# Kernel tuning notes

Measured on AMD Instinct MI355X. Metric: run time of the kernel, lower is better.

## Reference

```python
import jax, jax.numpy as jnp
import numpy as np

D = 512      # dgm / hidden width
L = 3        # n_dgm_layers
B = 131072   # collocation batch
SCALE = 0.02 # init scale to keep gates unsaturated


def setup_inputs() -> dict:
    key = jax.random.key(0)
    ks = jax.random.split(key, 12)
    X = jax.random.normal(ks[0], (B, 2), jnp.float32)
    t = jax.random.uniform(ks[1], (B, 1), jnp.float32)
    # input layer: Linear(3, D)
    W_in = jax.random.normal(ks[2], (3, D), jnp.float32) * SCALE
    b_in = jnp.zeros((D,), jnp.float32)
    # dense hidden: Linear(D, D)
    W_h1 = jax.random.normal(ks[3], (D, D), jnp.float32) * SCALE
    b_h1 = jnp.zeros((D,), jnp.float32)
    # projection to dgm dims: Linear(D, D)
    W_hd = jax.random.normal(ks[4], (D, D), jnp.float32) * SCALE
    b_hd = jnp.zeros((D,), jnp.float32)
    # DGM layers: 12 linears each, order [Uz,Wz,Bz, Ug,Wg,Bg, Ur,Wr,Br, Uh,Wh,Bh]
    dgm_W = jax.random.normal(ks[5], (L, 12, D, D), jnp.float32) * SCALE
    dgm_b = jnp.zeros((L, 12, D), jnp.float32)
    # output head: Linear(D, 1)
    W_out = jax.random.normal(ks[6], (D, 1), jnp.float32) * SCALE
    b_out = jnp.zeros((1,), jnp.float32)
    return {"X": X, "t": t, "W_in": W_in, "b_in": b_in, "W_h1": W_h1,
            "b_h1": b_h1, "W_hd": W_hd, "b_hd": b_hd, "dgm_W": dgm_W,
            "dgm_b": dgm_b, "W_out": W_out, "b_out": b_out}


def reference(X, t, W_in, b_in, W_h1, b_h1, W_hd, b_hd, dgm_W, dgm_b, W_out, b_out):
    inp = jnp.concatenate([X, t], axis=1)          # [B, 3]
    x = jnp.tanh(inp @ W_in + b_in)                # input layer + tanh
    x = jnp.tanh(x @ W_h1 + b_h1)                  # hidden Linear + tanh
    x = x @ W_hd + b_hd                            # hidden -> dgm projection (no act)
    S1 = x
    S = x
    for l in range(L):                             # small fixed layer loop
        W = dgm_W[l]
        b = dgm_b[l]
        lin = lambda i, v: v @ W[i] + b[i]
        Z = jax.nn.sigmoid(lin(0, x) + lin(1, S) + lin(2, S1))
        G = jax.nn.sigmoid(lin(3, x) + lin(4, S1) + lin(5, S))
        R = jax.nn.sigmoid(lin(6, x) + lin(7, S) + lin(8, S1))
        H = jnp.tanh(lin(9, x) + lin(10, S * R) + lin(11, S1))
        S = (1.0 - G) * H + Z * S
    return S @ W_out + b_out                       # [B, 1]
```

## Files before the change

### kernel.cpp

```cpp
#include <hip/hip_runtime.h>
#include <stdint.h>

namespace {

constexpr int B_ROWS = 131072;

typedef __attribute__((ext_vector_type(8))) short bf16x8;
typedef __attribute__((ext_vector_type(4))) float f32x4;

__device__ __forceinline__ unsigned short f2bf(float f) {
  unsigned u = __builtin_bit_cast(unsigned, f);
  u += 0x7fffu + ((u >> 16) & 1u);
  return (unsigned short)(u >> 16);
}
__device__ __forceinline__ float bf2f(unsigned short h) {
  unsigned u = ((unsigned)h) << 16;
  return __builtin_bit_cast(float, u);
}
__device__ __forceinline__ float sigm(float v) { return 1.0f / (1.0f + __expf(-v)); }


__global__ void pack_t_k(const float* __restrict__ W, unsigned short* __restrict__ Wt) {
  int idx = blockIdx.x * 256 + threadIdx.x;
  int n = idx >> 9, k = idx & 511;
  Wt[idx] = f2bf(W[(k << 9) + n]);
}

__global__ void pack_zgr_k(const float* __restrict__ dgmW, unsigned short* __restrict__ Wt) {
  long idx = (long)blockIdx.x * 256 + threadIdx.x;
  int l = (int)(idx / (1536 * 1024));
  int rest = (int)(idx - (long)l * (1536 * 1024));
  int n = rest >> 10, k = rest & 1023;
  int g = n >> 9, nn = n & 511;
  const int xi0[3] = {0, 3, 6};
  const int xi1[3] = {2, 4, 8};
  const int si[3] = {1, 5, 7};
  float v;
  if (k < 512)
    v = dgmW[(((long)(l * 12 + xi0[g]) << 9) + k) * 512 + nn] +
        dgmW[(((long)(l * 12 + xi1[g]) << 9) + k) * 512 + nn];
  else
    v = dgmW[(((long)(l * 12 + si[g]) << 9) + (k - 512)) * 512 + nn];
  Wt[idx] = f2bf(v);
}

__global__ void pack_h_k(const float* __restrict__ dgmW, unsigned short* __restrict__ Wt) {
  long idx = (long)blockIdx.x * 256 + threadIdx.x;
  int l = (int)(idx / (512 * 1024));
  int rest = (int)(idx - (long)l * (512 * 1024));
  int n = rest >> 10, k = rest & 1023;
  float v;
  if (k < 512)
    v = dgmW[(((long)(l * 12 + 9) << 9) + k) * 512 + n] +
        dgmW[(((long)(l * 12 + 11) << 9) + k) * 512 + n];
  else
    v = dgmW[(((long)(l * 12 + 10) << 9) + (k - 512)) * 512 + n];
  Wt[idx] = f2bf(v);
}

__global__ void pack_bias_k(const float* __restrict__ dgmb, float* __restrict__ bzgr,
                            float* __restrict__ bh) {
  int idx = blockIdx.x * 256 + threadIdx.x;
  if (idx >= 3 * 2048) return;
  int l = idx >> 11, n = idx & 2047;
  const float* bl = dgmb + l * 12 * 512;
  if (n < 1536) {
    int g = n >> 9, nn = n & 511;
    bzgr[l * 1536 + n] =
        bl[(g * 3 + 0) * 512 + nn] + bl[(g * 3 + 1) * 512 + nn] + bl[(g * 3 + 2) * 512 + nn];
  } else {
    int nn = n - 1536;
    bh[l * 512 + nn] = bl[9 * 512 + nn] + bl[10 * 512 + nn] + bl[11 * 512 + nn];
  }
}

__global__ void front0_k(const float* __restrict__ X, const float* __restrict__ t,
                         const float* __restrict__ Win, const float* __restrict__ bin,
                         unsigned short* __restrict__ x0, long row0) {
  long idx = (long)blockIdx.x * 256 + threadIdx.x;
  long r = idx >> 9;
  int c = (int)(idx & 511);
  long gr = row0 + r;
  float a = X[gr * 2] * Win[c] + X[gr * 2 + 1] * Win[512 + c] + t[gr] * Win[1024 + c] + bin[c];
  x0[idx] = f2bf(tanhf(a));
}

__global__ void head_k(const unsigned short* __restrict__ S, const float* __restrict__ Wout,
                       const float* __restrict__ bout, float* __restrict__ out, long row0) {
  const int lane = threadIdx.x & 63, wid = threadIdx.x >> 6;
  const long r = (long)blockIdx.x * 4 + wid;
  bf16x8 sv = *(const bf16x8*)&S[r * 512 + lane * 8];
  float sum = 0.f;
#pragma unroll
  for (int i = 0; i < 8; ++i) sum += bf2f((unsigned short)sv[i]) * Wout[lane * 8 + i];
#pragma unroll
  for (int off = 32; off > 0; off >>= 1) sum += __shfl_down(sum, off);
  if (lane == 0) out[row0 + r] = sum + bout[0];
}

template <int EPI, int KTILES>
__global__ __launch_bounds__(256, 2) void gemm_k(
    const unsigned short* __restrict__ a0, const unsigned short* __restrict__ a1,
    const unsigned short* __restrict__ wt, const float* __restrict__ bias,
    unsigned short* __restrict__ o0, unsigned short* __restrict__ o1,
    unsigned short* __restrict__ o2, const unsigned short* __restrict__ e0,
    const unsigned short* __restrict__ e1) {
  constexpr int K = KTILES * 64;
  __shared__ __align__(16) unsigned short As[128 * 64];
  __shared__ __align__(16) unsigned short Bs[128 * 64];
  const int tid = threadIdx.x;
  const int lane = tid & 63;
  const int wid = tid >> 6;
  const int wm = wid >> 1, wn = wid & 1;
  const long brow = (long)blockIdx.y * 128;
  const int bcol = blockIdx.x * 128;
  f32x4 acc[4][4] = {};

  for (int kt = 0; kt < KTILES; ++kt) {
    const unsigned short* asrc = (kt < 8) ? a0 : a1;
    const int kloc = (kt & 7) * 64;
    __syncthreads();
#pragma unroll
    for (int i = 0; i < 4; ++i) {
      const int c = tid + 256 * i;
      const int r = c >> 3, k8 = (c & 7) * 8;
      __builtin_amdgcn_global_load_lds(
          (const __attribute__((address_space(1))) void*)(asrc + (brow + r) * 512 + kloc + k8),
          (__attribute__((address_space(3))) void*)(&As[c * 8]), 16, 0, 0);
      __builtin_amdgcn_global_load_lds(
          (const __attribute__((address_space(1))) void*)(wt + (long)(bcol + r) * K + kt * 64 + k8),
          (__attribute__((address_space(3))) void*)(&Bs[c * 8]), 16, 0, 0);
    }
    __syncthreads();
#pragma unroll
    for (int ks = 0; ks < 2; ++ks) {
      bf16x8 af[4], bfv[4];
#pragma unroll
      for (int m = 0; m < 4; ++m)
        af[m] = *(const bf16x8*)&As[(wm * 64 + m * 16 + (lane & 15)) * 64 + ks * 32 + (lane >> 4) * 8];
#pragma unroll
      for (int n = 0; n < 4; ++n)
        bfv[n] = *(const bf16x8*)&Bs[(wn * 64 + n * 16 + (lane & 15)) * 64 + ks * 32 + (lane >> 4) * 8];
#pragma unroll
      for (int m = 0; m < 4; ++m)
#pragma unroll
        for (int n = 0; n < 4; ++n)
          acc[m][n] = __builtin_amdgcn_mfma_f32_16x16x32_bf16(af[m], bfv[n], acc[m][n], 0, 0, 0);
    }
  }

  const int g = bcol >> 9;
#pragma unroll
  for (int m = 0; m < 4; ++m) {
#pragma unroll
    for (int n = 0; n < 4; ++n) {
      const int col = bcol + wn * 64 + n * 16 + (lane & 15);
      const float bs = bias[col];
#pragma unroll
      for (int j = 0; j < 4; ++j) {
        const long row = brow + wm * 64 + m * 16 + (lane >> 4) * 4 + j;
        float v = acc[m][n][j] + bs;
        if constexpr (EPI == 0) {
          o0[row * 512 + col] = f2bf(tanhf(v));
        } else if constexpr (EPI == 1) {
          unsigned short b = f2bf(v);
          o0[row * 512 + col] = b;
          o1[row * 512 + col] = b;
        } else if constexpr (EPI == 2) {
          const int nn = col & 511;
          const float sgv = sigm(v);
          if (g == 0) {
            o0[row * 512 + nn] = f2bf(sgv * bf2f(e0[row * 512 + nn]));
          } else if (g == 1) {
            o1[row * 512 + nn] = f2bf(1.0f - sgv);
          } else {
            o2[row * 512 + nn] = f2bf(sgv * bf2f(e0[row * 512 + nn]));
          }
        } else {
          const float h = tanhf(v);
          const float omg = bf2f(e0[row * 512 + col]);
          const float zs = bf2f(e1[row * 512 + col]);
          o0[row * 512 + col] = f2bf(omg * h + zs);
        }
      }
    }
  }
}

}

extern "C" void kernel_launch(void* const* d_in, const int* in_sizes, int n_in,
                              void* d_out, int out_size, void* d_ws, size_t ws_size,
                              hipStream_t stream) {
  const float* X = (const float*)d_in[0];
  const float* t = (const float*)d_in[1];
  const float* W_in = (const float*)d_in[2];
  const float* b_in = (const float*)d_in[3];
  const float* W_h1 = (const float*)d_in[4];
  const float* b_h1 = (const float*)d_in[5];
  const float* W_hd = (const float*)d_in[6];
  const float* b_hd = (const float*)d_in[7];
  const float* dgm_W = (const float*)d_in[8];
  const float* dgm_b = (const float*)d_in[9];
  const float* W_out = (const float*)d_in[10];
  const float* b_out = (const float*)d_in[11];
  float* out = (float*)d_out;
  char* ws = (char*)d_ws;

  size_t off = 0;
  auto alloc = [&](size_t bytes) {
    size_t o = off;
    off = (off + bytes + 255) & ~(size_t)255;
    return o;
  };
  size_t o_wth1 = alloc((size_t)512 * 512 * 2);
  size_t o_wthd = alloc((size_t)512 * 512 * 2);
  size_t o_wtzgr = alloc((size_t)3 * 1536 * 1024 * 2);
  size_t o_wth = alloc((size_t)3 * 512 * 1024 * 2);
  size_t o_bzgr = alloc((size_t)3 * 1536 * 4);
  size_t o_bh = alloc((size_t)3 * 512 * 4);
  size_t actoff = off;

  unsigned short* wth1 = (unsigned short*)(ws + o_wth1);
  unsigned short* wthd = (unsigned short*)(ws + o_wthd);
  unsigned short* wtzgr = (unsigned short*)(ws + o_wtzgr);
  unsigned short* wth = (unsigned short*)(ws + o_wth);
  float* bzgr = (float*)(ws + o_bzgr);
  float* bh = (float*)(ws + o_bh);

  size_t avail = ws_size > actoff ? ws_size - actoff : 0;
  int nch = 1;
  while (nch < 1024 && (size_t)(B_ROWS / nch) * 512 * 2 * 5 > avail) nch <<= 1;
  const int R = B_ROWS / nch;
  unsigned short* xb = (unsigned short*)(ws + actoff);
  unsigned short* Sb = xb + (size_t)R * 512;
  unsigned short* ZSb = Sb + (size_t)R * 512;
  unsigned short* OGb = ZSb + (size_t)R * 512;
  unsigned short* SRb = OGb + (size_t)R * 512;

  pack_t_k<<<1024, 256, 0, stream>>>(W_h1, wth1);
  pack_t_k<<<1024, 256, 0, stream>>>(W_hd, wthd);
  pack_zgr_k<<<18432, 256, 0, stream>>>(dgm_W, wtzgr);
  pack_h_k<<<6144, 256, 0, stream>>>(dgm_W, wth);
  pack_bias_k<<<24, 256, 0, stream>>>(dgm_b, bzgr, bh);

  for (int c = 0; c < nch; ++c) {
    long row0 = (long)c * R;
    dim3 g4(4, R / 128), g12(12, R / 128);
    front0_k<<<R * 2, 256, 0, stream>>>(X, t, W_in, b_in, ZSb, row0);
    gemm_k<0, 8><<<g4, 256, 0, stream>>>(ZSb, nullptr, wth1, b_h1, OGb, nullptr, nullptr,
                                         nullptr, nullptr);
    gemm_k<1, 8><<<g4, 256, 0, stream>>>(OGb, nullptr, wthd, b_hd, xb, Sb, nullptr,
                                         nullptr, nullptr);
    for (int l = 0; l < 3; ++l) {
      gemm_k<2, 16><<<g12, 256, 0, stream>>>(xb, Sb, wtzgr + (size_t)l * 1536 * 1024,
                                             bzgr + l * 1536, ZSb, OGb, SRb, Sb, nullptr);
      gemm_k<3, 16><<<g4, 256, 0, stream>>>(xb, SRb, wth + (size_t)l * 512 * 1024,
                                            bh + l * 512, Sb, nullptr, nullptr, OGb, ZSb);
    }
    head_k<<<R / 4, 256, 0, stream>>>(Sb, W_out, b_out, out, row0);
  }
}
```

Baseline: 3.627 ms.

## Replace GEMM with 256x256-tile, 8-wave double-buffered pipelined kernel with XCD remap

Rewrites the bf16 MFMA GEMM to use 256x256 output tiles with 512 threads and 128KB of dynamic LDS, double-buffered across k-tiles. Loads are split into half-k stages and interleaved with the MFMA quarters, with explicit barriers, waitcnts and setprio. It adds an XOR swizzle on the LDS layout to avoid bank conflicts and remaps workgroups so each XCD gets contiguous tiles. The goal is more reuse per loaded byte and hiding global-load latency. The cost is fewer workgroups, higher register pressure from 32 accumulators per lane, and fragile hand scheduling.

```diff
diff --git a/kernel.cpp b/kernel.cpp
--- a/kernel.cpp
+++ b/kernel.cpp
@@ -99,66 +99,154 @@
 }
 
 template <int EPI, int KTILES>
-__global__ __launch_bounds__(256, 2) void gemm_k(
+__global__ __launch_bounds__(512, 2) void gemm8_k(
     const unsigned short* __restrict__ a0, const unsigned short* __restrict__ a1,
     const unsigned short* __restrict__ wt, const float* __restrict__ bias,
     unsigned short* __restrict__ o0, unsigned short* __restrict__ o1,
     unsigned short* __restrict__ o2, const unsigned short* __restrict__ e0,
     const unsigned short* __restrict__ e1) {
   constexpr int K = KTILES * 64;
-  __shared__ __align__(16) unsigned short As[128 * 64];
-  __shared__ __align__(16) unsigned short Bs[128 * 64];
+  constexpr int NT = KTILES;
+  extern __shared__ unsigned short lds[];
   const int tid = threadIdx.x;
   const int lane = tid & 63;
   const int wid = tid >> 6;
-  const int wm = wid >> 1, wn = wid & 1;
-  const long brow = (long)blockIdx.y * 128;
-  const int bcol = blockIdx.x * 128;
-  f32x4 acc[4][4] = {};
-
-  for (int kt = 0; kt < KTILES; ++kt) {
-    const unsigned short* asrc = (kt < 8) ? a0 : a1;
-    const int kloc = (kt & 7) * 64;
-    __syncthreads();
-#pragma unroll
-    for (int i = 0; i < 4; ++i) {
-      const int c = tid + 256 * i;
-      const int r = c >> 3, k8 = (c & 7) * 8;
-      __builtin_amdgcn_global_load_lds(
-          (const __attribute__((address_space(1))) void*)(asrc + (brow + r) * 512 + kloc + k8),
-          (__attribute__((address_space(3))) void*)(&As[c * 8]), 16, 0, 0);
-      __builtin_amdgcn_global_load_lds(
-          (const __attribute__((address_space(1))) void*)(wt + (long)(bcol + r) * K + kt * 64 + k8),
-          (__attribute__((address_space(3))) void*)(&Bs[c * 8]), 16, 0, 0);
-    }
-    __syncthreads();
-#pragma unroll
-    for (int ks = 0; ks < 2; ++ks) {
-      bf16x8 af[4], bfv[4];
-#pragma unroll
-      for (int m = 0; m < 4; ++m)
-        af[m] = *(const bf16x8*)&As[(wm * 64 + m * 16 + (lane & 15)) * 64 + ks * 32 + (lane >> 4) * 8];
-#pragma unroll
-      for (int n = 0; n < 4; ++n)
-        bfv[n] = *(const bf16x8*)&Bs[(wn * 64 + n * 16 + (lane & 15)) * 64 + ks * 32 + (lane >> 4) * 8];
-#pragma unroll
-      for (int m = 0; m < 4; ++m)
-#pragma unroll
-        for (int n = 0; n < 4; ++n)
-          acc[m][n] = __builtin_amdgcn_mfma_f32_16x16x32_bf16(af[m], bfv[n], acc[m][n], 0, 0, 0);
-    }
+  const int wm = wid >> 2, wn = wid & 3;
+
+  const int gx = gridDim.x;
+  const int nwg = gx * (int)gridDim.y;
+  const int orig = (int)blockIdx.y * gx + (int)blockIdx.x;
+  const int q = nwg >> 3, rr = nwg & 7;
+  const int xcd = orig & 7, lo = orig >> 3;
+  const int wg = ((xcd < rr) ? xcd * (q + 1) : rr * (q + 1) + (xcd - rr) * q) + lo;
+  const long brow = (long)(wg / gx) * 256;
+  const int bcol = (wg % gx) * 256;
+
+  f32x4 acc[8][4] = {};
+  bf16x8 af[4], bf[4];
+
+#define STAGE_A(db, kt, ks_)                                                                   \
+  do {                                                                                         \
+    const unsigned short* _src = ((kt) < 8) ? a0 : a1;                                         \
+    const int _koff = (((kt)&7) << 6) + (ks_)*32;                                              \
+    _Pragma("unroll") for (int _i = 0; _i < 2; ++_i) {                                         \
+      const int _c = tid + (_i << 9);                                                          \
+      const int _r = _c >> 2;                                                                  \
+      const int _gl = (_c & 3) ^ ((_r >> 1) & 3);                                              \
+      __builtin_amdgcn_global_load_lds(                                                        \
+          (const __attribute__((address_space(1))) void*)(_src + (brow + _r) * 512 + _koff +   \
+                                                          _gl * 8),                            \
+          (__attribute__((address_space(3))) void*)(lds + (db)*32768 + (ks_)*8192 + _c * 8),   \
+          16, 0, 0);                                                                           \
+    }                                                                                          \
+  } while (0)
+
+#define STAGE_B(db, kt, ks_)                                                                   \
+  do {                                                                                         \
+    _Pragma("unroll") for (int _i = 0; _i < 2; ++_i) {                                         \
+      const int _c = tid + (_i << 9);                                                          \
+      const int _r = _c >> 2;                                                                  \
+      const int _gl = (_c & 3) ^ ((_r >> 1) & 3);                                              \
+      __builtin_amdgcn_global_load_lds(                                                        \
+          (const __attribute__((address_space(1))) void*)(wt + (size_t)(bcol + _r) * K +       \
+                                                          ((kt) << 6) + (ks_)*32 + _gl * 8),   \
+          (__attribute__((address_space(3))) void*)(lds + (db)*32768 + 16384 + (ks_)*8192 +    \
+                                                    _c * 8),                                   \
+          16, 0, 0);                                                                           \
+    }                                                                                          \
+  } while (0)
+
+#define LOAD_A(mh, ks_)                                                                        \
+  do {                                                                                         \
+    _Pragma("unroll") for (int _m = 0; _m < 4; ++_m) {                                         \
+      const int _row = wm * 128 + ((mh)*4 + _m) * 16 + (lane & 15);                            \
+      const int _gp = (lane >> 4) ^ ((_row >> 1) & 3);                                         \
+      af[_m] = *(const bf16x8*)(lds + cb * 32768 + (ks_)*8192 + _row * 32 + _gp * 8);          \
+    }                                                                                          \
+  } while (0)
+
+#define LOAD_B(ks_)                                                                            \
+  do {                                                                                         \
+    _Pragma("unroll") for (int _n = 0; _n < 4; ++_n) {                                         \
+      const int _row = wn * 64 + _n * 16 + (lane & 15);                                        \
+      const int _gp = (lane >> 4) ^ ((_row >> 1) & 3);                                         \
+      bf[_n] = *(const bf16x8*)(lds + cb * 32768 + 16384 + (ks_)*8192 + _row * 32 + _gp * 8);  \
+    }                                                                                          \
+  } while (0)
+
+#define BAR_IN()                                          \
+  do {                                                    \
+    __builtin_amdgcn_s_barrier();                         \
+    asm volatile("s_waitcnt lgkmcnt(0)" ::: "memory");    \
+    __builtin_amdgcn_sched_barrier(0);                    \
+  } while (0)
+
+#define MFMA_Q(mh)                                                                             \
+  do {                                                                                         \
+    __builtin_amdgcn_s_setprio(1);                                                             \
+    _Pragma("unroll") for (int _m = 0; _m < 4; ++_m) _Pragma("unroll") for (int _n = 0;        \
+                                                                            _n < 4; ++_n)      \
+        acc[(mh)*4 + _m][_n] = __builtin_amdgcn_mfma_f32_16x16x32_bf16(                        \
+            af[_m], bf[_n], acc[(mh)*4 + _m][_n], 0, 0, 0);                                    \
+    __builtin_amdgcn_s_setprio(0);                                                             \
+  } while (0)
+
+  STAGE_A(0, 0, 0);
+  STAGE_B(0, 0, 0);
+  STAGE_A(0, 0, 1);
+  STAGE_B(0, 0, 1);
+  STAGE_B(1, 1, 0);
+  STAGE_A(1, 1, 0);
+  STAGE_B(1, 1, 1);
+  asm volatile("s_waitcnt vmcnt(6)" ::: "memory");
+  __builtin_amdgcn_s_barrier();
+
+  for (int t = 0; t < NT; ++t) {
+    const int cb = t & 1;
+    LOAD_B(0);
+    LOAD_A(0, 0);
+    if (t + 1 < NT) STAGE_A(cb ^ 1, t + 1, 1);
+    BAR_IN();
+    MFMA_Q(0);
+    __builtin_amdgcn_s_barrier();
+    LOAD_A(1, 0);
+    if (t + 2 < NT) STAGE_B(cb, t + 2, 0);
+    BAR_IN();
+    MFMA_Q(1);
+    __builtin_amdgcn_s_barrier();
+    LOAD_B(1);
+    LOAD_A(0, 1);
+    if (t + 2 < NT) STAGE_A(cb, t + 2, 0);
+    BAR_IN();
+    MFMA_Q(0);
+    __builtin_amdgcn_s_barrier();
+    LOAD_A(1, 1);
+    if (t + 2 < NT) STAGE_B(cb, t + 2, 1);
+    BAR_IN();
+    MFMA_Q(1);
+    if (t >= NT - 2)
+      asm volatile("s_waitcnt vmcnt(0)" ::: "memory");
+    else
+      asm volatile("s_waitcnt vmcnt(6)" ::: "memory");
+    __builtin_amdgcn_s_barrier();
   }
 
-  const int g = bcol >> 9;
-#pragma unroll
-  for (int m = 0; m < 4; ++m) {
+#undef STAGE_A
+#undef STAGE_B
+#undef LOAD_A
+#undef LOAD_B
+#undef BAR_IN
+#undef MFMA_Q
+
+#pragma unroll
+  for (int m = 0; m < 8; ++m) {
 #pragma unroll
     for (int n = 0; n < 4; ++n) {
       const int col = bcol + wn * 64 + n * 16 + (lane & 15);
       const float bs = bias[col];
 #pragma unroll
       for (int j = 0; j < 4; ++j) {
-        const long row = brow + wm * 64 + m * 16 + (lane >> 4) * 4 + j;
+        const long row = brow + wm * 128 + m * 16 + (lane >> 4) * 4 + j;
         float v = acc[m][n][j] + bs;
         if constexpr (EPI == 0) {
           o0[row * 512 + col] = f2bf(tanhf(v));
@@ -167,6 +255,7 @@
           o0[row * 512 + col] = b;
           o1[row * 512 + col] = b;
         } else if constexpr (EPI == 2) {
+          const int g = col >> 9;
           const int nn = col & 511;
           const float sgv = sigm(v);
           if (g == 0) {
@@ -207,6 +296,15 @@
   float* out = (float*)d_out;
   char* ws = (char*)d_ws;
 
+  (void)hipFuncSetAttribute((const void*)&gemm8_k<0, 8>,
+                            hipFuncAttributeMaxDynamicSharedMemorySize, 131072);
+  (void)hipFuncSetAttribute((const void*)&gemm8_k<1, 8>,
+                            hipFuncAttributeMaxDynamicSharedMemorySize, 131072);
+  (void)hipFuncSetAttribute((const void*)&gemm8_k<2, 16>,
+                            hipFuncAttributeMaxDynamicSharedMemorySize, 131072);
+  (void)hipFuncSetAttribute((const void*)&gemm8_k<3, 16>,
+                            hipFuncAttributeMaxDynamicSharedMemorySize, 131072);
+
   size_t off = 0;
   auto alloc = [&](size_t bytes) {
     size_t o = off;
@@ -230,7 +328,7 @@
 
   size_t avail = ws_size > actoff ? ws_size - actoff : 0;
   int nch = 1;
-  while (nch < 1024 && (size_t)(B_ROWS / nch) * 512 * 2 * 5 > avail) nch <<= 1;
+  while (nch < 512 && (size_t)(B_ROWS / nch) * 512 * 2 * 5 > avail) nch <<= 1;
   const int R = B_ROWS / nch;
   unsigned short* xb = (unsigned short*)(ws + actoff);
   unsigned short* Sb = xb + (size_t)R * 512;
@@ -246,17 +344,17 @@
 
   for (int c = 0; c < nch; ++c) {
     long row0 = (long)c * R;
-    dim3 g4(4, R / 128), g12(12, R / 128);
+    dim3 g2(2, R / 256), g6(6, R / 256);
     front0_k<<<R * 2, 256, 0, stream>>>(X, t, W_in, b_in, ZSb, row0);
-    gemm_k<0, 8><<<g4, 256, 0, stream>>>(ZSb, nullptr, wth1, b_h1, OGb, nullptr, nullptr,
-                                         nullptr, nullptr);
-    gemm_k<1, 8><<<g4, 256, 0, stream>>>(OGb, nullptr, wthd, b_hd, xb, Sb, nullptr,
-                                         nullptr, nullptr);
+    gemm8_k<0, 8><<<g2, 512, 131072, stream>>>(ZSb, ZSb, wth1, b_h1, OGb, nullptr, nullptr,
+                                               nullptr, nullptr);
+    gemm8_k<1, 8><<<g2, 512, 131072, stream>>>(OGb, OGb, wthd, b_hd, xb, Sb, nullptr,
+                                               nullptr, nullptr);
     for (int l = 0; l < 3; ++l) {
-      gemm_k<2, 16><<<g12, 256, 0, stream>>>(xb, Sb, wtzgr + (size_t)l * 1536 * 1024,
-                                             bzgr + l * 1536, ZSb, OGb, SRb, Sb, nullptr);
-      gemm_k<3, 16><<<g4, 256, 0, stream>>>(xb, SRb, wth + (size_t)l * 512 * 1024,
-                                            bh + l * 512, Sb, nullptr, nullptr, OGb, ZSb);
+      gemm8_k<2, 16><<<g6, 512, 131072, stream>>>(xb, Sb, wtzgr + (size_t)l * 1536 * 1024,
+                                                  bzgr + l * 1536, ZSb, OGb, SRb, Sb, nullptr);
+      gemm8_k<3, 16><<<g2, 512, 131072, stream>>>(xb, SRb, wth + (size_t)l * 512 * 1024,
+                                                  bh + l * 512, Sb, nullptr, nullptr, OGb, ZSb);
     }
     head_k<<<R / 4, 256, 0, stream>>>(Sb, W_out, b_out, out, row0);
   }
```

After: 3.376 ms. 6.9% less time.

## Keep full-K weight slab resident in LDS and stream activations from global

Applied to the files above, without the earlier changes.

Replaces the 128x128 double-sync LDS GEMM with a 512-row by 64-column tile per 512-thread workgroup. The whole K-extent of the weight slice is loaded once into XOR-swizzled dynamic LDS, and activations are read directly from global memory with no per-k-tile barriers. Workgroups are remapped so each XCD gets a contiguous range of tiles. The intent is to remove the per-tile sync and LDS staging cost for A. In exchange it uses up to 128KB of LDS, which limits occupancy, and A loads go uncached through global/L2.

```diff
diff --git a/kernel.cpp b/kernel.cpp
--- a/kernel.cpp
+++ b/kernel.cpp
@@ -98,67 +98,85 @@
   if (lane == 0) out[row0 + r] = sum + bout[0];
 }
 
-template <int EPI, int KTILES>
-__global__ __launch_bounds__(256, 2) void gemm_k(
+template <int EPI, int KHALVES>
+__global__ __launch_bounds__(512, 2) void gemmN64_k(
     const unsigned short* __restrict__ a0, const unsigned short* __restrict__ a1,
     const unsigned short* __restrict__ wt, const float* __restrict__ bias,
     unsigned short* __restrict__ o0, unsigned short* __restrict__ o1,
     unsigned short* __restrict__ o2, const unsigned short* __restrict__ e0,
     const unsigned short* __restrict__ e1) {
-  constexpr int K = KTILES * 64;
-  __shared__ __align__(16) unsigned short As[128 * 64];
-  __shared__ __align__(16) unsigned short Bs[128 * 64];
+  constexpr int K = KHALVES * 512;
+  constexpr int K8 = K / 8;
+  extern __shared__ unsigned short lds[];
   const int tid = threadIdx.x;
-  const int lane = tid & 63;
-  const int wid = tid >> 6;
-  const int wm = wid >> 1, wn = wid & 1;
-  const long brow = (long)blockIdx.y * 128;
-  const int bcol = blockIdx.x * 128;
+
+  const int gx = gridDim.x;
+  const int nwg = gx * (int)gridDim.y;
+  const int orig = (int)blockIdx.y * gx + (int)blockIdx.x;
+  const int q = nwg >> 3, rr = nwg & 7;
+  const int xcd = orig & 7, lo = orig >> 3;
+  const int wg = ((xcd < rr) ? xcd * (q + 1) : rr * (q + 1) + (xcd - rr) * q) + lo;
+  const long brow = (long)(wg / gx) * 512;
+  const int bcol = (wg % gx) * 64;
+
+#pragma unroll
+  for (int i = 0; i < (64 * K8) / 512; ++i) {
+    const int c = tid + (i << 9);
+    const int col = c / K8, k8 = c % K8;
+    bf16x8 v = *(const bf16x8*)(wt + (size_t)(bcol + col) * K + k8 * 8);
+    *(bf16x8*)(lds + col * K + ((k8 ^ (col & 7)) << 3)) = v;
+  }
+  __syncthreads();
+
+  const int lane = tid & 63, w = tid >> 6;
+  const int lr = lane & 15, kk = lane >> 4;
+  const long rbase = brow + w * 64 + lr;
   f32x4 acc[4][4] = {};
 
-  for (int kt = 0; kt < KTILES; ++kt) {
-    const unsigned short* asrc = (kt < 8) ? a0 : a1;
-    const int kloc = (kt & 7) * 64;
-    __syncthreads();
-#pragma unroll
-    for (int i = 0; i < 4; ++i) {
-      const int c = tid + 256 * i;
-      const int r = c >> 3, k8 = (c & 7) * 8;
-      __builtin_amdgcn_global_load_lds(
-          (const __attribute__((address_space(1))) void*)(asrc + (brow + r) * 512 + kloc + k8),
-          (__attribute__((address_space(3))) void*)(&As[c * 8]), 16, 0, 0);
-      __builtin_amdgcn_global_load_lds(
-          (const __attribute__((address_space(1))) void*)(wt + (long)(bcol + r) * K + kt * 64 + k8),
-          (__attribute__((address_space(3))) void*)(&Bs[c * 8]), 16, 0, 0);
+#pragma unroll
+  for (int kh = 0; kh < KHALVES; ++kh) {
+    const unsigned short* __restrict__ asrc = kh ? a1 : a0;
+#pragma unroll 4
+    for (int ks = 0; ks < 16; ++ks) {
+      const int kw = ks * 32 + kk * 8;
+      const int k8g = kh * 64 + ks * 4 + kk;
+      const int bko = ((k8g ^ (lr & 7)) << 3);
+      bf16x8 af0 = *(const bf16x8*)(asrc + (rbase + 0) * 512 + kw);
+      bf16x8 af1 = *(const bf16x8*)(asrc + (rbase + 16) * 512 + kw);
+      bf16x8 af2 = *(const bf16x8*)(asrc + (rbase + 32) * 512 + kw);
+      bf16x8 af3 = *(const bf16x8*)(asrc + (rbase + 48) * 512 + kw);
+      bf16x8 bf0 = *(const bf16x8*)(lds + (0 * 16 + lr) * K + bko);
+      bf16x8 bf1 = *(const bf16x8*)(lds + (1 * 16 + lr) * K + bko);
+      bf16x8 bf2 = *(const bf16x8*)(lds + (2 * 16 + lr) * K + bko);
+      bf16x8 bf3 = *(const bf16x8*)(lds + (3 * 16 + lr) * K + bko);
+      acc[0][0] = __builtin_amdgcn_mfma_f32_16x16x32_bf16(af0, bf0, acc[0][0], 0, 0, 0);
+      acc[0][1] = __builtin_amdgcn_mfma_f32_16x16x32_bf16(af0, bf1, acc[0][1], 0, 0, 0);
+      acc[0][2] = __builtin_amdgcn_mfma_f32_16x16x32_bf16(af0, bf2, acc[0][2], 0, 0, 0);
+      acc[0][3] = __builtin_amdgcn_mfma_f32_16x16x32_bf16(af0, bf3, acc[0][3], 0, 0, 0);
+      acc[1][0] = __builtin_amdgcn_mfma_f32_16x16x32_bf16(af1, bf0, acc[1][0], 0, 0, 0);
+      acc[1][1] = __builtin_amdgcn_mfma_f32_16x16x32_bf16(af1, bf1, acc[1][1], 0, 0, 0);
+      acc[1][2] = __builtin_amdgcn_mfma_f32_16x16x32_bf16(af1, bf2, acc[1][2], 0, 0, 0);
+      acc[1][3] = __builtin_amdgcn_mfma_f32_16x16x32_bf16(af1, bf3, acc[1][3], 0, 0, 0);
+      acc[2][0] = __builtin_amdgcn_mfma_f32_16x16x32_bf16(af2, bf0, acc[2][0], 0, 0, 0);
+      acc[2][1] = __builtin_amdgcn_mfma_f32_16x16x32_bf16(af2, bf1, acc[2][1], 0, 0, 0);
+      acc[2][2] = __builtin_amdgcn_mfma_f32_16x16x32_bf16(af2, bf2, acc[2][2], 0, 0, 0);
+      acc[2][3] = __builtin_amdgcn_mfma_f32_16x16x32_bf16(af2, bf3, acc[2][3], 0, 0, 0);
+      acc[3][0] = __builtin_amdgcn_mfma_f32_16x16x32_bf16(af3, bf0, acc[3][0], 0, 0, 0);
+      acc[3][1] = __builtin_amdgcn_mfma_f32_16x16x32_bf16(af3, bf1, acc[3][1], 0, 0, 0);
+      acc[3][2] = __builtin_amdgcn_mfma_f32_16x16x32_bf16(af3, bf2, acc[3][2], 0, 0, 0);
+      acc[3][3] = __builtin_amdgcn_mfma_f32_16x16x32_bf16(af3, bf3, acc[3][3], 0, 0, 0);
     }
-    __syncthreads();
-#pragma unroll
-    for (int ks = 0; ks < 2; ++ks) {
-      bf16x8 af[4], bfv[4];
-#pragma unroll
-      for (int m = 0; m < 4; ++m)
-        af[m] = *(const bf16x8*)&As[(wm * 64 + m * 16 + (lane & 15)) * 64 + ks * 32 + (lane >> 4) * 8];
-#pragma unroll
-      for (int n = 0; n < 4; ++n)
-        bfv[n] = *(const bf16x8*)&Bs[(wn * 64 + n * 16 + (lane & 15)) * 64 + ks * 32 + (lane >> 4) * 8];
-#pragma unroll
-      for (int m = 0; m < 4; ++m)
-#pragma unroll
-        for (int n = 0; n < 4; ++n)
-          acc[m][n] = __builtin_amdgcn_mfma_f32_16x16x32_bf16(af[m], bfv[n], acc[m][n], 0, 0, 0);
-    }
-  }
-
-  const int g = bcol >> 9;
+  }
+
 #pragma unroll
   for (int m = 0; m < 4; ++m) {
 #pragma unroll
     for (int n = 0; n < 4; ++n) {
-      const int col = bcol + wn * 64 + n * 16 + (lane & 15);
+      const int col = bcol + n * 16 + lr;
       const float bs = bias[col];
 #pragma unroll
       for (int j = 0; j < 4; ++j) {
-        const long row = brow + wm * 64 + m * 16 + (lane >> 4) * 4 + j;
+        const long row = brow + w * 64 + m * 16 + kk * 4 + j;
         float v = acc[m][n][j] + bs;
         if constexpr (EPI == 0) {
           o0[row * 512 + col] = f2bf(tanhf(v));
@@ -167,6 +185,7 @@
           o0[row * 512 + col] = b;
           o1[row * 512 + col] = b;
         } else if constexpr (EPI == 2) {
+          const int g = col >> 9;
           const int nn = col & 511;
           const float sgv = sigm(v);
           if (g == 0) {
@@ -207,6 +226,15 @@
   float* out = (float*)d_out;
   char* ws = (char*)d_ws;
 
+  (void)hipFuncSetAttribute((const void*)&gemmN64_k<0, 1>,
+                            hipFuncAttributeMaxDynamicSharedMemorySize, 65536);
+  (void)hipFuncSetAttribute((const void*)&gemmN64_k<1, 1>,
+                            hipFuncAttributeMaxDynamicSharedMemorySize, 65536);
+  (void)hipFuncSetAttribute((const void*)&gemmN64_k<2, 2>,
+                            hipFuncAttributeMaxDynamicSharedMemorySize, 131072);
+  (void)hipFuncSetAttribute((const void*)&gemmN64_k<3, 2>,
+                            hipFuncAttributeMaxDynamicSharedMemorySize, 131072);
+
   size_t off = 0;
   auto alloc = [&](size_t bytes) {
     size_t o = off;
@@ -230,7 +258,7 @@
 
   size_t avail = ws_size > actoff ? ws_size - actoff : 0;
   int nch = 1;
-  while (nch < 1024 && (size_t)(B_ROWS / nch) * 512 * 2 * 5 > avail) nch <<= 1;
+  while (nch < 256 && (size_t)(B_ROWS / nch) * 512 * 2 * 5 > avail) nch <<= 1;
   const int R = B_ROWS / nch;
   unsigned short* xb = (unsigned short*)(ws + actoff);
   unsigned short* Sb = xb + (size_t)R * 512;
@@ -246,17 +274,17 @@
 
   for (int c = 0; c < nch; ++c) {
     long row0 = (long)c * R;
-    dim3 g4(4, R / 128), g12(12, R / 128);
+    dim3 g8(8, R / 512), g24(24, R / 512);
     front0_k<<<R * 2, 256, 0, stream>>>(X, t, W_in, b_in, ZSb, row0);
-    gemm_k<0, 8><<<g4, 256, 0, stream>>>(ZSb, nullptr, wth1, b_h1, OGb, nullptr, nullptr,
-                                         nullptr, nullptr);
-    gemm_k<1, 8><<<g4, 256, 0, stream>>>(OGb, nullptr, wthd, b_hd, xb, Sb, nullptr,
-                                         nullptr, nullptr);
+    gemmN64_k<0, 1><<<g8, 512, 65536, stream>>>(ZSb, ZSb, wth1, b_h1, OGb, nullptr, nullptr,
+                                                nullptr, nullptr);
+    gemmN64_k<1, 1><<<g8, 512, 65536, stream>>>(OGb, OGb, wthd, b_hd, xb, Sb, nullptr,
+                                                nullptr, nullptr);
     for (int l = 0; l < 3; ++l) {
-      gemm_k<2, 16><<<g12, 256, 0, stream>>>(xb, Sb, wtzgr + (size_t)l * 1536 * 1024,
-                                             bzgr + l * 1536, ZSb, OGb, SRb, Sb, nullptr);
-      gemm_k<3, 16><<<g4, 256, 0, stream>>>(xb, SRb, wth + (size_t)l * 512 * 1024,
-                                            bh + l * 512, Sb, nullptr, nullptr, OGb, ZSb);
+      gemmN64_k<2, 2><<<g24, 512, 131072, stream>>>(xb, Sb, wtzgr + (size_t)l * 1536 * 1024,
+                                                    bzgr + l * 1536, ZSb, OGb, SRb, Sb, nullptr);
+      gemmN64_k<3, 2><<<g8, 512, 131072, stream>>>(xb, SRb, wth + (size_t)l * 512 * 1024,
+                                                   bh + l * 512, Sb, nullptr, nullptr, OGb, ZSb);
     }
     head_k<<<R / 4, 256, 0, stream>>>(Sb, W_out, b_out, out, row0);
   }
```

New measurement: 4.917 ms. 1.36x slower.

## Replace GEMM with persistent 256x256 double-buffered pipelined MFMA kernel

Applied to the files above, without the earlier changes.

Replaces the 128x128 single-buffered GEMM with a persistent kernel of 512 threads. Each block takes a contiguous run of 256x256 output tiles and remaps block IDs so that neighbouring jobs land on the same XCD. Loads go directly into LDS through a swizzled, double-buffered ring, with explicit vmcnt waits, barriers and setprio interleaving the MFMA work with prefetch of the next stage. The aim is to hide global-load latency, raise arithmetic intensity per LDS byte and cut launch and tail overhead. In exchange it needs 128KB of dynamic LDS, which may limit occupancy, and the hand-written barrier and waitcnt schedule is fragile.

```diff
diff --git a/kernel.cpp b/kernel.cpp
--- a/kernel.cpp
+++ b/kernel.cpp
@@ -98,89 +98,174 @@
   if (lane == 0) out[row0 + r] = sum + bout[0];
 }
 
-template <int EPI, int KTILES>
-__global__ __launch_bounds__(256, 2) void gemm_k(
+template <int EPI, int KT, int LOGKT, int NCOL>
+__global__ __launch_bounds__(512, 2) void gemmP_k(
     const unsigned short* __restrict__ a0, const unsigned short* __restrict__ a1,
     const unsigned short* __restrict__ wt, const float* __restrict__ bias,
     unsigned short* __restrict__ o0, unsigned short* __restrict__ o1,
     unsigned short* __restrict__ o2, const unsigned short* __restrict__ e0,
-    const unsigned short* __restrict__ e1) {
-  constexpr int K = KTILES * 64;
-  __shared__ __align__(16) unsigned short As[128 * 64];
-  __shared__ __align__(16) unsigned short Bs[128 * 64];
+    const unsigned short* __restrict__ e1, int njobs, int jpb) {
+  constexpr int K = KT * 64;
+  extern __shared__ unsigned short lds[];
   const int tid = threadIdx.x;
-  const int lane = tid & 63;
-  const int wid = tid >> 6;
-  const int wm = wid >> 1, wn = wid & 1;
-  const long brow = (long)blockIdx.y * 128;
-  const int bcol = blockIdx.x * 128;
-  f32x4 acc[4][4] = {};
-
-  for (int kt = 0; kt < KTILES; ++kt) {
-    const unsigned short* asrc = (kt < 8) ? a0 : a1;
-    const int kloc = (kt & 7) * 64;
-    __syncthreads();
-#pragma unroll
-    for (int i = 0; i < 4; ++i) {
-      const int c = tid + 256 * i;
-      const int r = c >> 3, k8 = (c & 7) * 8;
-      __builtin_amdgcn_global_load_lds(
-          (const __attribute__((address_space(1))) void*)(asrc + (brow + r) * 512 + kloc + k8),
-          (__attribute__((address_space(3))) void*)(&As[c * 8]), 16, 0, 0);
-      __builtin_amdgcn_global_load_lds(
-          (const __attribute__((address_space(1))) void*)(wt + (long)(bcol + r) * K + kt * 64 + k8),
-          (__attribute__((address_space(3))) void*)(&Bs[c * 8]), 16, 0, 0);
-    }
-    __syncthreads();
-#pragma unroll
-    for (int ks = 0; ks < 2; ++ks) {
-      bf16x8 af[4], bfv[4];
-#pragma unroll
-      for (int m = 0; m < 4; ++m)
-        af[m] = *(const bf16x8*)&As[(wm * 64 + m * 16 + (lane & 15)) * 64 + ks * 32 + (lane >> 4) * 8];
+  const int lane = tid & 63, wid = tid >> 6;
+  const int wm = wid >> 2, wn = wid & 3;
+  const int lr = lane & 15, kk = lane >> 4;
+
+  const int G = gridDim.x;
+  const int q = G >> 3, rr = G & 7;
+  const int xcd = (int)blockIdx.x & 7, lo = (int)blockIdx.x >> 3;
+  const int bsw = ((xcd < rr) ? xcd * (q + 1) : rr * (q + 1) + (xcd - rr) * q) + lo;
+  const int j0 = bsw * jpb;
+  if (j0 >= njobs) return;
+  const int nj = min(jpb, njobs - j0);
+  const int nseq = nj << LOGKT;
+
+  const int gp8 = ((kk ^ ((lr >> 1) & 3)) << 3);
+  const int a_rd = (wm * 128 + lr) * 32 + gp8;
+  const int b_rd = 16384 + (wn * 64 + lr) * 32 + gp8;
+  const int r0 = tid >> 2, gl0 = (tid & 3) ^ ((r0 >> 1) & 3);
+  const int c1 = tid + 512, r1 = c1 >> 2, gl1 = (c1 & 3) ^ ((r1 >> 1) & 3);
+  const int aL0 = r0 * 512 + gl0 * 8, aL1 = r1 * 512 + gl1 * 8;
+  const size_t bL0 = (size_t)r0 * K + gl0 * 8, bL1 = (size_t)r1 * K + gl1 * 8;
+  const int dL0 = tid * 8, dL1 = (tid + 512) * 8;
+
+  f32x4 acc[8][4] = {};
+  bf16x8 af[4], bf[4];
+
+  auto stA = [&](int s2, int ks) {
+    if (s2 >= nseq) return;
+    const int jj = j0 + (s2 >> LOGKT);
+    const int mt = jj / NCOL;
+    const int kt2 = s2 & (KT - 1);
+    const unsigned short* src = (KT == 16 && (kt2 & 8)) ? a1 : a0;
+    const long pb = (long)mt * 131072 + (kt2 & 7) * 64 + ks * 32;
+    const int d = ((s2 & 1) << 15) + ks * 8192;
+    __builtin_amdgcn_global_load_lds(
+        (const __attribute__((address_space(1))) void*)(src + pb + aL0),
+        (__attribute__((address_space(3))) void*)(lds + d + dL0), 16, 0, 0);
+    __builtin_amdgcn_global_load_lds(
+        (const __attribute__((address_space(1))) void*)(src + pb + aL1),
+        (__attribute__((address_space(3))) void*)(lds + d + dL1), 16, 0, 0);
+  };
+  auto stB = [&](int s2, int ks) {
+    if (s2 >= nseq) return;
+    const int jj = j0 + (s2 >> LOGKT);
+    const int col = jj % NCOL;
+    const int kt2 = s2 & (KT - 1);
+    const size_t pb = (size_t)col * (256 * K) + kt2 * 64 + ks * 32;
+    const int d = ((s2 & 1) << 15) + 16384 + ks * 8192;
+    __builtin_amdgcn_global_load_lds(
+        (const __attribute__((address_space(1))) void*)(wt + pb + bL0),
+        (__attribute__((address_space(3))) void*)(lds + d + dL0), 16, 0, 0);
+    __builtin_amdgcn_global_load_lds(
+        (const __attribute__((address_space(1))) void*)(wt + pb + bL1),
+        (__attribute__((address_space(3))) void*)(lds + d + dL1), 16, 0, 0);
+  };
+  auto ldA = [&](int cbo, int mh, int ks) {
+#pragma unroll
+    for (int m = 0; m < 4; ++m)
+      af[m] = *(const bf16x8*)(lds + cbo + ks * 8192 + a_rd + mh * 2048 + m * 512);
+  };
+  auto ldB = [&](int cbo, int ks) {
+#pragma unroll
+    for (int n = 0; n < 4; ++n)
+      bf[n] = *(const bf16x8*)(lds + cbo + ks * 8192 + b_rd + n * 512);
+  };
+  auto mmq = [&](int mh) {
+    __builtin_amdgcn_s_setprio(1);
+#pragma unroll
+    for (int m = 0; m < 4; ++m)
 #pragma unroll
       for (int n = 0; n < 4; ++n)
-        bfv[n] = *(const bf16x8*)&Bs[(wn * 64 + n * 16 + (lane & 15)) * 64 + ks * 32 + (lane >> 4) * 8];
-#pragma unroll
-      for (int m = 0; m < 4; ++m)
-#pragma unroll
-        for (int n = 0; n < 4; ++n)
-          acc[m][n] = __builtin_amdgcn_mfma_f32_16x16x32_bf16(af[m], bfv[n], acc[m][n], 0, 0, 0);
-    }
-  }
-
-  const int g = bcol >> 9;
-#pragma unroll
-  for (int m = 0; m < 4; ++m) {
-#pragma unroll
-    for (int n = 0; n < 4; ++n) {
-      const int col = bcol + wn * 64 + n * 16 + (lane & 15);
-      const float bs = bias[col];
-#pragma unroll
-      for (int j = 0; j < 4; ++j) {
-        const long row = brow + wm * 64 + m * 16 + (lane >> 4) * 4 + j;
-        float v = acc[m][n][j] + bs;
-        if constexpr (EPI == 0) {
-          o0[row * 512 + col] = f2bf(tanhf(v));
-        } else if constexpr (EPI == 1) {
-          unsigned short b = f2bf(v);
-          o0[row * 512 + col] = b;
-          o1[row * 512 + col] = b;
-        } else if constexpr (EPI == 2) {
-          const int nn = col & 511;
-          const float sgv = sigm(v);
-          if (g == 0) {
-            o0[row * 512 + nn] = f2bf(sgv * bf2f(e0[row * 512 + nn]));
-          } else if (g == 1) {
-            o1[row * 512 + nn] = f2bf(1.0f - sgv);
-          } else {
-            o2[row * 512 + nn] = f2bf(sgv * bf2f(e0[row * 512 + nn]));
+        acc[mh * 4 + m][n] =
+            __builtin_amdgcn_mfma_f32_16x16x32_bf16(af[m], bf[n], acc[mh * 4 + m][n], 0, 0, 0);
+    __builtin_amdgcn_s_setprio(0);
+  };
+
+  stB(0, 0);
+  stA(0, 0);
+  stB(0, 1);
+  stA(0, 1);
+  stB(1, 0);
+  stA(1, 0);
+  stB(1, 1);
+  asm volatile("s_waitcnt vmcnt(5)" ::: "memory");
+  __builtin_amdgcn_s_barrier();
+
+  for (int s = 0; s < nseq; ++s) {
+    const int cbo = (s & 1) << 15;
+    const bool deep = (s + 4 <= nseq);
+    ldB(cbo, 0);
+    ldA(cbo, 0, 0);
+    stA(s + 1, 1);
+    __builtin_amdgcn_s_barrier();
+    mmq(0);
+    __builtin_amdgcn_s_barrier();
+    ldA(cbo, 1, 0);
+    stB(s + 2, 0);
+    __builtin_amdgcn_s_barrier();
+    mmq(1);
+    if (deep)
+      asm volatile("s_waitcnt vmcnt(5)" ::: "memory");
+    else
+      asm volatile("s_waitcnt vmcnt(0)" ::: "memory");
+    __builtin_amdgcn_s_barrier();
+    ldB(cbo, 1);
+    ldA(cbo, 0, 1);
+    stA(s + 2, 0);
+    __builtin_amdgcn_s_barrier();
+    mmq(0);
+    __builtin_amdgcn_s_barrier();
+    ldA(cbo, 1, 1);
+    stB(s + 2, 1);
+    __builtin_amdgcn_s_barrier();
+    mmq(1);
+    if (deep)
+      asm volatile("s_waitcnt vmcnt(5)" ::: "memory");
+    else
+      asm volatile("s_waitcnt vmcnt(0)" ::: "memory");
+    __builtin_amdgcn_s_barrier();
+
+    if ((s & (KT - 1)) == (KT - 1)) {
+      const int jj = j0 + (s >> LOGKT);
+      const long brow = (long)(jj / NCOL) * 256;
+      const int bcol = (jj % NCOL) * 256;
+#pragma unroll
+      for (int m = 0; m < 8; ++m) {
+#pragma unroll
+        for (int n = 0; n < 4; ++n) {
+          const int col = bcol + wn * 64 + n * 16 + lr;
+          const float bs = bias[col];
+#pragma unroll
+          for (int j = 0; j < 4; ++j) {
+            const long row = brow + wm * 128 + m * 16 + kk * 4 + j;
+            float v = acc[m][n][j] + bs;
+            if constexpr (EPI == 0) {
+              o0[row * 512 + col] = f2bf(tanhf(v));
+            } else if constexpr (EPI == 1) {
+              unsigned short b = f2bf(v);
+              o0[row * 512 + col] = b;
+              o1[row * 512 + col] = b;
+            } else if constexpr (EPI == 2) {
+              const int g = col >> 9;
+              const int nn = col & 511;
+              const float sgv = sigm(v);
+              if (g == 0) {
+                o0[row * 512 + nn] = f2bf(sgv * bf2f(e0[row * 512 + nn]));
+              } else if (g == 1) {
+                o1[row * 512 + nn] = f2bf(1.0f - sgv);
+              } else {
+                o2[row * 512 + nn] = f2bf(sgv * bf2f(e0[row * 512 + nn]));
+              }
+            } else {
+              const float h = tanhf(v);
+              const float omg = bf2f(e0[row * 512 + col]);
+              const float zs = bf2f(e1[row * 512 + col]);
+              o0[row * 512 + col] = f2bf(omg * h + zs);
+            }
+            acc[m][n][j] = 0.0f;
           }
-        } else {
-          const float h = tanhf(v);
-          const float omg = bf2f(e0[row * 512 + col]);
-          const float zs = bf2f(e1[row * 512 + col]);
-          o0[row * 512 + col] = f2bf(omg * h + zs);
         }
       }
     }
@@ -207,6 +292,15 @@
   float* out = (float*)d_out;
   char* ws = (char*)d_ws;
 
+  (void)hipFuncSetAttribute((const void*)&gemmP_k<0, 8, 3, 2>,
+                            hipFuncAttributeMaxDynamicSharedMemorySize, 131072);
+  (void)hipFuncSetAttribute((const void*)&gemmP_k<1, 8, 3, 2>,
+                            hipFuncAttributeMaxDynamicSharedMemorySize, 131072);
+  (void)hipFuncSetAttribute((const void*)&gemmP_k<2, 16, 4, 6>,
+                            hipFuncAttributeMaxDynamicSharedMemorySize, 131072);
+  (void)hipFuncSetAttribute((const void*)&gemmP_k<3, 16, 4, 2>,
+                            hipFuncAttributeMaxDynamicSharedMemorySize, 131072);
+
   size_t off = 0;
   auto alloc = [&](size_t bytes) {
     size_t o = off;
@@ -230,7 +324,7 @@
 
   size_t avail = ws_size > actoff ? ws_size - actoff : 0;
   int nch = 1;
-  while (nch < 1024 && (size_t)(B_ROWS / nch) * 512 * 2 * 5 > avail) nch <<= 1;
+  while (nch < 256 && (size_t)(B_ROWS / nch) * 512 * 2 * 5 > avail) nch <<= 1;
   const int R = B_ROWS / nch;
   unsigned short* xb = (unsigned short*)(ws + actoff);
   unsigned short* Sb = xb + (size_t)R * 512;
@@ -244,19 +338,30 @@
   pack_h_k<<<6144, 256, 0, stream>>>(dgm_W, wth);
   pack_bias_k<<<24, 256, 0, stream>>>(dgm_b, bzgr, bh);
 
+  const int MT = R / 256;
+  auto cfg = [](int njobs, int& jpb, int& G) {
+    jpb = (njobs + 255) / 256;
+    G = (njobs + jpb - 1) / jpb;
+  };
+  int nj2 = 2 * MT, jpb2, G2;
+  cfg(nj2, jpb2, G2);
+  int nj6 = 6 * MT, jpb6, G6;
+  cfg(nj6, jpb6, G6);
+
   for (int c = 0; c < nch; ++c) {
     long row0 = (long)c * R;
-    dim3 g4(4, R / 128), g12(12, R / 128);
     front0_k<<<R * 2, 256, 0, stream>>>(X, t, W_in, b_in, ZSb, row0);
-    gemm_k<0, 8><<<g4, 256, 0, stream>>>(ZSb, nullptr, wth1, b_h1, OGb, nullptr, nullptr,
-                                         nullptr, nullptr);
-    gemm_k<1, 8><<<g4, 256, 0, stream>>>(OGb, nullptr, wthd, b_hd, xb, Sb, nullptr,
-                                         nullptr, nullptr);
+    gemmP_k<0, 8, 3, 2><<<G2, 512, 131072, stream>>>(ZSb, ZSb, wth1, b_h1, OGb, nullptr,
+                                                     nullptr, nullptr, nullptr, nj2, jpb2);
+    gemmP_k<1, 8, 3, 2><<<G2, 512, 131072, stream>>>(OGb, OGb, wthd, b_hd, xb, Sb, nullptr,
+                                                     nullptr, nullptr, nj2, jpb2);
     for (int l = 0; l < 3; ++l) {
-      gemm_k<2, 16><<<g12, 256, 0, stream>>>(xb, Sb, wtzgr + (size_t)l * 1536 * 1024,
-                                             bzgr + l * 1536, ZSb, OGb, SRb, Sb, nullptr);
-      gemm_k<3, 16><<<g4, 256, 0, stream>>>(xb, SRb, wth + (size_t)l * 512 * 1024,
-                                            bh + l * 512, Sb, nullptr, nullptr, OGb, ZSb);
+      gemmP_k<2, 16, 4, 6><<<G6, 512, 131072, stream>>>(
+          xb, Sb, wtzgr + (size_t)l * 1536 * 1024, bzgr + l * 1536, ZSb, OGb, SRb, Sb,
+          nullptr, nj6, jpb6);
+      gemmP_k<3, 16, 4, 2><<<G2, 512, 131072, stream>>>(
+          xb, SRb, wth + (size_t)l * 512 * 1024, bh + l * 512, Sb, nullptr, nullptr, OGb,
+          ZSb, nj2, jpb2);
     }
     head_k<<<R / 4, 256, 0, stream>>>(Sb, W_out, b_out, out, row0);
   }
```

Result: faster. 3.419 ms (-5.7%).
